# Kernel optimization log

Measured on AMD Instinct MI355X. Metric: run time of the kernel, lower is better.

The kernel has to match this reference:

```python
import jax, jax.numpy as jnp
import numpy as np

N = 50000       # nodes
E = 1600000     # edges (avg degree 32)
F_IN = 128      # input node features
HID = 64        # hidden_dim
H = 2           # heads in conv1
NEG_SLOPE = 0.2 # PyG GATConv default


def gat_conv(x, W, a_src, a_dst, b, src, dst, heads, out_ch):
    """PyG-style GATConv (concat=True). x:[n,f], W:[f,heads*out_ch],
    a_src/a_dst:[heads,out_ch], b:[heads*out_ch], src/dst:[e]."""
    n = x.shape[0]
    xh = (x @ W).reshape(n, heads, out_ch)              # [n,H,C]
    s_src = jnp.sum(xh * a_src[None], axis=-1)          # [n,H]
    s_dst = jnp.sum(xh * a_dst[None], axis=-1)          # [n,H]
    e = jax.nn.leaky_relu(s_src[src] + s_dst[dst], NEG_SLOPE)  # [e,H]
    # segment softmax over incoming edges of each destination node
    emax = jax.ops.segment_max(e, dst, num_segments=n)  # [n,H]
    emax = jnp.where(jnp.isfinite(emax), emax, 0.0)
    p = jnp.exp(e - emax[dst])
    denom = jax.ops.segment_sum(p, dst, num_segments=n)
    alpha = p / (denom[dst] + 1e-16)                    # [e,H]
    out = jax.ops.segment_sum(xh[src] * alpha[..., None], dst, num_segments=n)
    return out.reshape(n, heads * out_ch) + b


def setup_inputs() -> dict:
    key = jax.random.key(0)
    ks = jax.random.split(key, 14)
    g = lambda k, shape, fan: jax.random.normal(k, shape, jnp.float32) / np.sqrt(fan).astype(np.float32)
    return {
        "x": jax.random.normal(ks[0], (N, F_IN), jnp.float32),
        "edge_index": jax.random.randint(ks[1], (2, E), 0, N, jnp.int32),
        "W1": g(ks[2], (F_IN, H * HID), F_IN),
        "a_src1": g(ks[3], (H, HID), HID),
        "a_dst1": g(ks[4], (H, HID), HID),
        "b1": jnp.zeros((H * HID,), jnp.float32),
        "W2": g(ks[5], (H * HID, HID), H * HID),
        "a_src2": g(ks[6], (1, HID), HID),
        "a_dst2": g(ks[7], (1, HID), HID),
        "b2": jnp.zeros((HID,), jnp.float32),
        "Wm": g(ks[8], (HID, 1), HID),
        "bm": jnp.zeros((1,), jnp.float32),
        "Wl": g(ks[9], (HID, 4), HID),
        "bl": jnp.zeros((4,), jnp.float32),
    }


def reference(x, edge_index, W1, a_src1, a_dst1, b1, W2, a_src2, a_dst2, b2, Wm, bm, Wl, bl):
    n = x.shape[0]
    loop = jnp.arange(n, dtype=edge_index.dtype)        # PyG add_self_loops=True
    src = jnp.concatenate([edge_index[0], loop])
    dst = jnp.concatenate([edge_index[1], loop])
    h = jax.nn.relu(gat_conv(x, W1, a_src1, a_dst1, b1, src, dst, H, HID))
    # dropout layers are identity in eval mode
    h = jax.nn.relu(gat_conv(h, W2, a_src2, a_dst2, b2, src, dst, 1, HID))
    mortality = h @ Wm + bm   # [n,1]
    los = h @ Wl + bl         # [n,4]
    return (mortality, los)
```

## Files before the change

kernel.cpp:

```cpp
#include <hip/hip_runtime.h>
#include <hip/hip_bf16.h>

typedef __hip_bfloat16 bf16;
typedef __attribute__((ext_vector_type(8))) short short8;
typedef __attribute__((ext_vector_type(4))) float f32x4;

static __device__ __forceinline__ float lrelu(float x){ return x > 0.f ? x : 0.2f * x; }

static __device__ __forceinline__ float ldf(const void* p, size_t i, int f32){
  return f32 ? ((const float*)p)[i] : __bfloat162float(((const bf16*)p)[i]);
}

static __device__ __forceinline__ float wsum(float v){
#pragma unroll
  for (int o = 32; o; o >>= 1) v += __shfl_xor(v, o, 64);
  return v;
}
static __device__ __forceinline__ float qsum(float v){
  v += __shfl_xor(v, 1); v += __shfl_xor(v, 2);
  v += __shfl_xor(v, 4); v += __shfl_xor(v, 8);
  return v;
}

static __device__ __forceinline__ unsigned short f2bf(float x){
  unsigned u = __float_as_uint(x);
  unsigned r = (u + 0x7fffu + ((u >> 16) & 1u)) >> 16;
  return (unsigned short)r;
}
static __device__ __forceinline__ float bfval(unsigned short h){
  return __uint_as_float(((unsigned)h) << 16);
}
static __device__ __forceinline__ unsigned packbf2(float a, float b){
  return ((unsigned)f2bf(b) << 16) | (unsigned)f2bf(a);
}
static __device__ __forceinline__ float unlo(unsigned v){ return __uint_as_float(v << 16); }
static __device__ __forceinline__ float unhi(unsigned v){ return __uint_as_float(v & 0xffff0000u); }

#define CAP 10240
#define EPB 16
#define CHUNK (256 * EPB)
#define PREPB 96
#define SORTCAP 9216

__global__ __launch_bounds__(256) void k_prep_scatter(
    const unsigned short* __restrict__ xprobe,
    const void* __restrict__ W1, const void* __restrict__ W2,
    int* __restrict__ flag,
    unsigned short* __restrict__ w1hi, unsigned short* __restrict__ w1lo,
    unsigned short* __restrict__ w2hi, unsigned short* __restrict__ w2lo,
    const int* __restrict__ ei, int* __restrict__ bucketCur,
    unsigned* __restrict__ binned, int E, int Etot){
  __shared__ int lcnt[256];
  __shared__ int lcur[256];
  int t = threadIdx.x;
  if (blockIdx.x < PREPB){
    if (t == 0) lcnt[0] = 0;
    __syncthreads();
    int bad = 0;
    for (int i = t; i < 512; i += 256){
      int e = (xprobe[i] >> 7) & 0xFF;
      if (e >= 133) bad++;
    }
    if (bad) atomicAdd(&lcnt[0], bad);
    __syncthreads();
    const int f = lcnt[0] > 8;
    if (blockIdx.x == 0 && t == 0) *flag = f;
    int blk = blockIdx.x;
    const void* W; unsigned short *hi, *lo; int ncol, nct, tg;
    if (blk < 64){ W = W1; hi = w1hi; lo = w1lo; ncol = 128; nct = 8; tg = blk * 256 + t; }
    else         { W = W2; hi = w2hi; lo = w2lo; ncol = 64;  nct = 4; tg = (blk - 64) * 256 + t; }
    int j = tg & 7;
    int lane = (tg >> 3) & 63;
    int ct = (tg >> 9) % nct;
    int kc = tg / (512 * nct);
    int k = kc * 32 + ((lane >> 4) << 3) + j;
    int col = ct * 16 + (lane & 15);
    float w = ldf(W, (size_t)k * ncol + col, f);
    unsigned short h = f2bf(w);
    hi[tg] = h;
    lo[tg] = f2bf(w - bfval(h));
  } else {
    lcnt[t] = 0;
    __syncthreads();
    int base = (blockIdx.x - PREPB) * CHUNK;
    int vsrc[EPB], vdst[EPB];
#pragma unroll
    for (int k = 0; k < EPB; k++){
      int i = base + k * 256 + t;
      vdst[k] = -1;
      if (i < Etot){
        if (i < E){ vsrc[k] = ei[i]; vdst[k] = ei[E + i]; }
        else { vsrc[k] = i - E; vdst[k] = i - E; }
        atomicAdd(&lcnt[vdst[k] >> 8], 1);
      }
    }
    __syncthreads();
    lcur[t] = lcnt[t] ? atomicAdd(&bucketCur[t], lcnt[t]) : 0;
    __syncthreads();
#pragma unroll
    for (int k = 0; k < EPB; k++){
      if (vdst[k] >= 0){
        int b = vdst[k] >> 8;
        int p = atomicAdd(&lcur[b], 1);
        binned[(size_t)b * CAP + p] = (unsigned)vsrc[k] | ((unsigned)(vdst[k] & 255) << 24);
      }
    }
  }
}

__global__ __launch_bounds__(256) void k_sort_gemm1(
    const int* __restrict__ bucketCur, const unsigned* __restrict__ binned,
    int* __restrict__ deg, int* __restrict__ offs, int* __restrict__ csr, int nbuck,
    const void* __restrict__ x,
    const unsigned short* __restrict__ whi, const unsigned short* __restrict__ wlo,
    const void* __restrict__ a_src1, const void* __restrict__ a_dst1,
    const int* __restrict__ flagp,
    unsigned* __restrict__ xh1p, float* __restrict__ ssrc1, float* __restrict__ sdst1, int n){
  __shared__ int smem[768 + SORTCAP];
  int t = threadIdx.x;
  if ((int)blockIdx.x < nbuck){
    int* lcnt = smem;
    int* lsc  = smem + 256;
    int* lcur = smem + 512;
    int* lsrc = smem + 768;
    int b = blockIdx.x;
    int s0 = b * CAP;
    int cnt = bucketCur[b];
    int node0 = b << 8;
    lcnt[t] = 0;
    __syncthreads();
    for (int i = t; i < cnt; i += 256){
      unsigned v = binned[s0 + i];
      atomicAdd(&lcnt[v >> 24], 1);
    }
    __syncthreads();
    lsc[t] = lcnt[t];
    __syncthreads();
#pragma unroll
    for (int o = 1; o < 256; o <<= 1){
      int xv = (t >= o) ? lsc[t - o] : 0;
      __syncthreads();
      lsc[t] += xv;
      __syncthreads();
    }
    int excl = lsc[t] - lcnt[t];
    int node = node0 + t;
    if (node < n){ deg[node] = lcnt[t]; offs[node] = s0 + excl; }
    lcur[t] = excl;
    __syncthreads();
    if (cnt <= SORTCAP){
      for (int i = t; i < cnt; i += 256){
        unsigned v = binned[s0 + i];
        int p = atomicAdd(&lcur[v >> 24], 1);
        lsrc[p] = (int)(v & 0xFFFFFFu);
      }
      __syncthreads();
      for (int i = t; i < cnt; i += 256) csr[s0 + i] = lsrc[i];
    } else {
      for (int i = t; i < cnt; i += 256){
        unsigned v = binned[s0 + i];
        int p = atomicAdd(&lcur[v >> 24], 1);
        csr[s0 + p] = (int)(v & 0xFFFFFFu);
      }
    }
  } else {
    const int f = *flagp;
    int lane = t & 63, w = t >> 6;
    int c16 = lane & 15, quad = lane >> 4;
    int nbw = (blockIdx.x - nbuck) * 64 + w * 16;
    int an = min(nbw + c16, n - 1);
    f32x4 acc[8];
#pragma unroll
    for (int ct = 0; ct < 8; ct++)
#pragma unroll
      for (int r = 0; r < 4; r++) acc[ct][r] = 0.f;

#pragma unroll
    for (int kc = 0; kc < 4; kc++){
      float av[8];
      short8 ahi, alo;
      if (f){
        const float* row = (const float*)x + (size_t)an * 128 + kc * 32 + quad * 8;
        float4 v0 = *(const float4*)row;
        float4 v1 = *(const float4*)(row + 4);
        av[0] = v0.x; av[1] = v0.y; av[2] = v0.z; av[3] = v0.w;
        av[4] = v1.x; av[5] = v1.y; av[6] = v1.z; av[7] = v1.w;
#pragma unroll
        for (int j = 0; j < 8; j++){
          unsigned short h = f2bf(av[j]);
          ahi[j] = (short)h;
          alo[j] = (short)f2bf(av[j] - bfval(h));
        }
      } else {
        const unsigned short* row = (const unsigned short*)x + (size_t)an * 128 + kc * 32 + quad * 8;
        uint4 v = *(const uint4*)row;
        ahi[0] = (short)(v.x & 0xffff); ahi[1] = (short)(v.x >> 16);
        ahi[2] = (short)(v.y & 0xffff); ahi[3] = (short)(v.y >> 16);
        ahi[4] = (short)(v.z & 0xffff); ahi[5] = (short)(v.z >> 16);
        ahi[6] = (short)(v.w & 0xffff); ahi[7] = (short)(v.w >> 16);
#pragma unroll
        for (int j = 0; j < 8; j++) alo[j] = 0;
      }
#pragma unroll
      for (int ct = 0; ct < 8; ct++){
        const short8 bhi = *(const short8*)(whi + (((size_t)(kc * 8 + ct) * 64 + lane) << 3));
        const short8 blo = *(const short8*)(wlo + (((size_t)(kc * 8 + ct) * 64 + lane) << 3));
        acc[ct] = __builtin_amdgcn_mfma_f32_16x16x32_bf16(ahi, blo, acc[ct], 0, 0, 0);
        acc[ct] = __builtin_amdgcn_mfma_f32_16x16x32_bf16(alo, bhi, acc[ct], 0, 0, 0);
        acc[ct] = __builtin_amdgcn_mfma_f32_16x16x32_bf16(ahi, bhi, acc[ct], 0, 0, 0);
      }
    }

    float as[8], ad[8];
#pragma unroll
    for (int ct = 0; ct < 8; ct++){
      as[ct] = ldf(a_src1, ct * 16 + c16, f);
      ad[ct] = ldf(a_dst1, ct * 16 + c16, f);
    }
    float vs0[4], vs1[4], vd0[4], vd1[4];
#pragma unroll
    for (int r = 0; r < 4; r++){
      float s0 = 0.f, s1 = 0.f, d0 = 0.f, d1 = 0.f;
#pragma unroll
      for (int ct = 0; ct < 4; ct++){
        s0 += acc[ct][r] * as[ct];         d0 += acc[ct][r] * ad[ct];
        s1 += acc[ct + 4][r] * as[ct + 4]; d1 += acc[ct + 4][r] * ad[ct + 4];
      }
      vs0[r] = qsum(s0); vs1[r] = qsum(s1);
      vd0[r] = qsum(d0); vd1[r] = qsum(d1);
    }
#pragma unroll
    for (int r = 0; r < 4; r++){
      int node = nbw + quad * 4 + r;
      if (node < n){
#pragma unroll
        for (int ct = 0; ct < 4; ct++)
          xh1p[(size_t)node * 64 + ct * 16 + c16] = packbf2(acc[ct][r], acc[ct + 4][r]);
      }
    }
    if (c16 == 0){
#pragma unroll
      for (int r = 0; r < 4; r++){
        int node = nbw + quad * 4 + r;
        if (node < n){
          ssrc1[node * 2]     = vs0[r];
          ssrc1[node * 2 + 1] = vs1[r];
          sdst1[node * 2]     = vd0[r];
          sdst1[node * 2 + 1] = vd1[r];
        }
      }
    }
  }
}

__global__ __launch_bounds__(256) void k_gemm2m(
    const unsigned* __restrict__ h1p,
    const unsigned short* __restrict__ whi, const unsigned short* __restrict__ wlo,
    const void* __restrict__ a_src2, const void* __restrict__ a_dst2,
    const int* __restrict__ flagp,
    unsigned short* __restrict__ xh2b, float* __restrict__ ssrc2, float* __restrict__ sdst2, int n){
  const int f = *flagp;
  int t = threadIdx.x;
  int lane = t & 63, w = t >> 6;
  int c16 = lane & 15, quad = lane >> 4;
  int nbw = blockIdx.x * 64 + w * 16;
  int an = min(nbw + c16, n - 1);
  f32x4 acc[4];
#pragma unroll
  for (int ct = 0; ct < 4; ct++)
#pragma unroll
    for (int r = 0; r < 4; r++) acc[ct][r] = 0.f;

#pragma unroll
  for (int kc = 0; kc < 4; kc++){
    const uint4* hp = (const uint4*)h1p;
    uint4 v = hp[(size_t)an * 16 + kc * 4 + quad];
    short8 ahi;
    ahi[0] = (short)(v.x & 0xffff); ahi[1] = (short)(v.x >> 16);
    ahi[2] = (short)(v.y & 0xffff); ahi[3] = (short)(v.y >> 16);
    ahi[4] = (short)(v.z & 0xffff); ahi[5] = (short)(v.z >> 16);
    ahi[6] = (short)(v.w & 0xffff); ahi[7] = (short)(v.w >> 16);
#pragma unroll
    for (int ct = 0; ct < 4; ct++){
      const short8 bhi = *(const short8*)(whi + (((size_t)(kc * 4 + ct) * 64 + lane) << 3));
      const short8 blo = *(const short8*)(wlo + (((size_t)(kc * 4 + ct) * 64 + lane) << 3));
      acc[ct] = __builtin_amdgcn_mfma_f32_16x16x32_bf16(ahi, blo, acc[ct], 0, 0, 0);
      acc[ct] = __builtin_amdgcn_mfma_f32_16x16x32_bf16(ahi, bhi, acc[ct], 0, 0, 0);
    }
  }

  float as[4], ad[4];
#pragma unroll
  for (int ct = 0; ct < 4; ct++){
    as[ct] = ldf(a_src2, ct * 16 + c16, f);
    ad[ct] = ldf(a_dst2, ct * 16 + c16, f);
  }
  float vs[4], vd[4];
#pragma unroll
  for (int r = 0; r < 4; r++){
    float s = 0.f, d = 0.f;
#pragma unroll
    for (int ct = 0; ct < 4; ct++){
      s += acc[ct][r] * as[ct];
      d += acc[ct][r] * ad[ct];
    }
    vs[r] = qsum(s); vd[r] = qsum(d);
  }
#pragma unroll
  for (int r = 0; r < 4; r++){
    int node = nbw + quad * 4 + r;
    if (node < n){
#pragma unroll
      for (int ct = 0; ct < 4; ct++)
        xh2b[(size_t)node * 64 + ct * 16 + c16] = f2bf(acc[ct][r]);
    }
  }
  if (c16 == 0){
#pragma unroll
    for (int r = 0; r < 4; r++){
      int node = nbw + quad * 4 + r;
      if (node < n){ ssrc2[node] = vs[r]; sdst2[node] = vd[r]; }
    }
  }
}

__global__ __launch_bounds__(256) void k_agg1(
    const int* __restrict__ offs, const int* __restrict__ deg, const int* __restrict__ csr,
    const float2* __restrict__ ssrc, const float2* __restrict__ sdst,
    const unsigned* __restrict__ xh1p, const void* __restrict__ b1,
    const int* __restrict__ flagp, unsigned* __restrict__ h1p, int n){
  __shared__ float4 stg[4][64];
  int wv = threadIdx.x >> 6;
  int wid = (int)(((size_t)blockIdx.x * blockDim.x + threadIdx.x) >> 6);
  int lane = threadIdx.x & 63;
  if (wid >= n) return;
  int st = offs[wid], d = deg[wid];
  int half = lane >> 5, u = lane & 31;
  float2 sd = sdst[wid];
  const char* __restrict__ xb = (const char*)xh1p;
  const unsigned uoff = (unsigned)u * 8u;
  float Z0l = 0.f, Z1l = 0.f;
  float a0x = 0.f, a0y = 0.f, a1x = 0.f, a1y = 0.f;
  for (int base = 0; base < d; base += 64){
    int idx = base + lane;
    bool val = idx < d;
    int s = csr[st + (val ? idx : 0)];
    float2 sv = ssrc[s];
    float e0 = fminf(lrelu(sv.x + sd.x), 80.f);
    float e1 = fminf(lrelu(sv.y + sd.y), 80.f);
    float p0 = val ? __expf(e0) : 0.f;
    float p1 = val ? __expf(e1) : 0.f;
    Z0l += p0; Z1l += p1;
    float4 tv; tv.x = __uint_as_float((unsigned)s); tv.y = p0; tv.z = p1; tv.w = 0.f;
    stg[wv][lane] = tv;
    int cnt = min(64, d - base);
    int pairs = (cnt + 1) >> 1;
    for (int pj = 0; pj < pairs; pj += 8){
      unsigned offv[8]; float q0v[8], q1v[8]; uint2 vv[8];
#pragma unroll
      for (int k = 0; k < 8; k++){
        int jj = ((pj + k) << 1) + half;
        float4 v = stg[wv][jj];
        offv[k] = (__float_as_uint(v.x) << 8) + uoff;
        q0v[k] = v.y;
        q1v[k] = v.z;
      }
#pragma unroll
      for (int k = 0; k < 8; k++)
        vv[k] = *(const uint2*)(xb + offv[k]);
#pragma unroll
      for (int k = 0; k < 8; k++){
        a0x = fmaf(q0v[k], unlo(vv[k].x), a0x); a0y = fmaf(q0v[k], unlo(vv[k].y), a0y);
        a1x = fmaf(q1v[k], unhi(vv[k].x), a1x); a1y = fmaf(q1v[k], unhi(vv[k].y), a1y);
      }
    }
  }
  a0x += __shfl_xor(a0x, 32); a0y += __shfl_xor(a0y, 32);
  a1x += __shfl_xor(a1x, 32); a1y += __shfl_xor(a1y, 32);
  float Z0 = wsum(Z0l), Z1 = wsum(Z1l);
  const int f = *flagp;
  float Zh = half ? Z1 : Z0;
  float ax = half ? a1x : a0x;
  float ay = half ? a1y : a0y;
  float inv = 1.f / (Zh + 1e-16f);
  float bx = ldf(b1, half * 64 + 2 * u, f);
  float by = ldf(b1, half * 64 + 2 * u + 1, f);
  float ox = fmaxf(ax * inv + bx, 0.f);
  float oy = fmaxf(ay * inv + by, 0.f);
  h1p[(size_t)wid * 64 + half * 32 + u] = packbf2(ox, oy);
}

__global__ __launch_bounds__(256) void k_agg2(
    const int* __restrict__ offs, const int* __restrict__ deg, const int* __restrict__ csr,
    const float* __restrict__ ssrc, const float* __restrict__ sdstA,
    const unsigned short* __restrict__ xh2b, const void* __restrict__ bias2,
    const void* __restrict__ Wm, const void* __restrict__ bm,
    const void* __restrict__ Wlos, const void* __restrict__ bl,
    const int* __restrict__ flagp, void* __restrict__ out, int n){
  __shared__ float2 stg[4][96];
  int wv = threadIdx.x >> 6;
  int wid = (int)(((size_t)blockIdx.x * blockDim.x + threadIdx.x) >> 6);
  int lane = threadIdx.x & 63;
  if (wid >= n) return;
  int st = offs[wid], d = deg[wid];
  int half = lane >> 5, u = lane & 31;
  if (lane < 32){ float2 z; z.x = __uint_as_float(0u); z.y = 0.f; stg[wv][64 + lane] = z; }
  float sd = sdstA[wid];
  const char* __restrict__ xb = (const char*)xh2b;
  const unsigned uoff = (unsigned)u * 4u;
  float Zl = 0.f, ax = 0.f, ay = 0.f;
  for (int base = 0; base < d; base += 64){
    int idx = base + lane;
    bool val = idx < d;
    int s = csr[st + (val ? idx : 0)];
    float e = fminf(lrelu(ssrc[s] + sd), 80.f);
    float p = val ? __expf(e) : 0.f;
    Zl += p;
    float2 tv; tv.x = __uint_as_float((unsigned)s); tv.y = p;
    stg[wv][lane] = tv;
    int cnt = min(64, d - base);
    int pairs = (cnt + 1) >> 1;
    for (int pj = 0; pj < pairs; pj += 12){
      unsigned offv[12]; float qv[12]; unsigned vv[12];
#pragma unroll
      for (int k = 0; k < 12; k++){
        int jj = ((pj + k) << 1) + half;
        float2 v = stg[wv][jj];
        offv[k] = (__float_as_uint(v.x) << 7) + uoff;
        qv[k] = v.y;
      }
#pragma unroll
      for (int k = 0; k < 12; k++)
        vv[k] = *(const unsigned*)(xb + offv[k]);
#pragma unroll
      for (int k = 0; k < 12; k++){
        ax = fmaf(qv[k], unlo(vv[k]), ax);
        ay = fmaf(qv[k], unhi(vv[k]), ay);
      }
    }
  }
  ax += __shfl_xor(ax, 32);
  ay += __shfl_xor(ay, 32);
  float Z = wsum(Zl);
  const int f = *flagp;
  float inv = 1.f / (Z + 1e-16f);
  float hx = fmaxf(ax * inv + ldf(bias2, 2 * u, f), 0.f);
  float hy = fmaxf(ay * inv + ldf(bias2, 2 * u + 1, f), 0.f);
  bool lo32 = (half == 0);
  float mo = wsum(lo32 ? hx * ldf(Wm, 2 * u, f) + hy * ldf(Wm, 2 * u + 1, f) : 0.f);
  float l0 = wsum(lo32 ? hx * ldf(Wlos, (2 * u) * 4 + 0, f) + hy * ldf(Wlos, (2 * u + 1) * 4 + 0, f) : 0.f);
  float l1 = wsum(lo32 ? hx * ldf(Wlos, (2 * u) * 4 + 1, f) + hy * ldf(Wlos, (2 * u + 1) * 4 + 1, f) : 0.f);
  float l2 = wsum(lo32 ? hx * ldf(Wlos, (2 * u) * 4 + 2, f) + hy * ldf(Wlos, (2 * u + 1) * 4 + 2, f) : 0.f);
  float l3 = wsum(lo32 ? hx * ldf(Wlos, (2 * u) * 4 + 3, f) + hy * ldf(Wlos, (2 * u + 1) * 4 + 3, f) : 0.f);
  if (lane == 0){
    float vm = mo + ldf(bm, 0, f);
    float v0 = l0 + ldf(bl, 0, f);
    float v1 = l1 + ldf(bl, 1, f);
    float v2 = l2 + ldf(bl, 2, f);
    float v3 = l3 + ldf(bl, 3, f);
    if (f){
      float* o = (float*)out;
      o[wid] = vm;
      float4 lv = make_float4(v0, v1, v2, v3);
      *(float4*)&o[n + wid * 4] = lv;
    } else {
      bf16* o = (bf16*)out;
      o[wid] = __float2bfloat16(vm);
      o[n + wid * 4 + 0] = __float2bfloat16(v0); o[n + wid * 4 + 1] = __float2bfloat16(v1);
      o[n + wid * 4 + 2] = __float2bfloat16(v2); o[n + wid * 4 + 3] = __float2bfloat16(v3);
    }
  }
}

extern "C" void kernel_launch(void* const* d_in, const int* in_sizes, int n_in,
                              void* d_out, int out_size, void* d_ws, size_t ws_size,
                              hipStream_t stream){
  const void* x      = d_in[0];
  const int*  ei     = (const int*)d_in[1];
  const void* W1     = d_in[2];
  const void* a_src1 = d_in[3];
  const void* a_dst1 = d_in[4];
  const void* b1     = d_in[5];
  const void* W2     = d_in[6];
  const void* a_src2 = d_in[7];
  const void* a_dst2 = d_in[8];
  const void* bias2  = d_in[9];
  const void* Wm     = d_in[10];
  const void* bm     = d_in[11];
  const void* Wlos   = d_in[12];
  const void* bl     = d_in[13];

  const int N = in_sizes[0] / 128;
  const int E = in_sizes[1] / 2;
  const int Etot = E + N;
  const int NBUCK = (N + 255) >> 8;

  char* base = (char*)d_ws;
  size_t off = 0;
  auto alloc = [&](size_t bytes) -> void* {
    void* r = base + off;
    off += (bytes + 255) & ~(size_t)255;
    return r;
  };
  int*      flag  = (int*)alloc(256);
  unsigned* xh1p  = (unsigned*)alloc((size_t)N * 64 * 4);
  unsigned* h1p   = (unsigned*)alloc((size_t)N * 64 * 4);
  float*    ssrc1 = (float*)alloc((size_t)N * 2 * 4);
  float*    sdst1 = (float*)alloc((size_t)N * 2 * 4);
  float*    ssrc2 = (float*)alloc((size_t)N * 4);
  float*    sdst2 = (float*)alloc((size_t)N * 4);
  int*      deg    = (int*)alloc((size_t)N * 4);
  int*      offsb  = (int*)alloc((size_t)N * 4);
  unsigned* binned = (unsigned*)alloc((size_t)NBUCK * CAP * 4);
  int*      csr    = (int*)alloc((size_t)NBUCK * CAP * 4);
  int*      bucketCur = (int*)alloc(1024);
  unsigned short* w1hi = (unsigned short*)alloc(16384 * 2);
  unsigned short* w1lo = (unsigned short*)alloc(16384 * 2);
  unsigned short* w2hi = (unsigned short*)alloc(8192 * 2);
  unsigned short* w2lo = (unsigned short*)alloc(8192 * 2);
  unsigned short* xh2b = (unsigned short*)xh1p;

  const int nchunk = (Etot + CHUNK - 1) / CHUNK;
  const int ngemm1 = (N + 63) / 64;

  hipMemsetAsync(bucketCur, 0, (size_t)NBUCK * 4, stream);

  k_prep_scatter<<<PREPB + nchunk, 256, 0, stream>>>(
      (const unsigned short*)x, W1, W2, flag, w1hi, w1lo, w2hi, w2lo,
      ei, bucketCur, binned, E, Etot);

  k_sort_gemm1<<<NBUCK + ngemm1, 256, 0, stream>>>(
      bucketCur, binned, deg, offsb, csr, NBUCK,
      x, w1hi, w1lo, a_src1, a_dst1, flag, xh1p, ssrc1, sdst1, N);

  k_agg1<<<(N + 3) / 4, 256, 0, stream>>>(offsb, deg, csr, (const float2*)ssrc1, (const float2*)sdst1,
                                          xh1p, b1, flag, h1p, N);

  k_gemm2m<<<(N + 63) / 64, 256, 0, stream>>>(h1p, w2hi, w2lo, a_src2, a_dst2, flag, xh2b, ssrc2, sdst2, N);
  k_agg2<<<(N + 3) / 4, 256, 0, stream>>>(offsb, deg, csr, ssrc2, sdst2, xh2b, bias2,
                                          Wm, bm, Wlos, bl, flag, d_out, N);
}
```

Measured before the change: 258.1 us.

## Split aggregation waves into quarter-waves with wide gathers and double-buffered loads

Both edge-aggregation kernels now give each quarter-wave its own edge, so every lane gathers 16 bytes (layer 1) or 8 bytes (layer 2) of the source row instead of 8 or 4. Loads for the next group of 16 edges are issued before the current group's FMAs run, a manual double-buffering meant to hide gather latency. Partial sums are reduced across quarters at the end, and launch bounds now request 8 blocks per CU. This targets latency and instruction overhead in the memory-bound gathers, at the cost of more registers per lane and an extra shuffle reduction.

```diff
diff --git a/kernel.cpp b/kernel.cpp
--- a/kernel.cpp
+++ b/kernel.cpp
@@ -324,7 +324,23 @@
   }
 }
 
-__global__ __launch_bounds__(256) void k_agg1(
+#define AG1_ISSUE(V0,V1,V2,V3,P) { \
+  int b0_ = ((P) << 4) + qd; \
+  V0 = *(const uint4*)(xb + ((__float_as_uint(stg[wv][b0_ +  0].x) << 8) + uoff)); \
+  V1 = *(const uint4*)(xb + ((__float_as_uint(stg[wv][b0_ +  4].x) << 8) + uoff)); \
+  V2 = *(const uint4*)(xb + ((__float_as_uint(stg[wv][b0_ +  8].x) << 8) + uoff)); \
+  V3 = *(const uint4*)(xb + ((__float_as_uint(stg[wv][b0_ + 12].x) << 8) + uoff)); }
+#define AG1_FMA1(V,SL) { \
+  float4 w_ = stg[wv][SL]; float q0_ = w_.y, q1_ = w_.z; \
+  a00 = fmaf(q0_, unlo(V.x), a00); a10 = fmaf(q1_, unhi(V.x), a10); \
+  a01 = fmaf(q0_, unlo(V.y), a01); a11 = fmaf(q1_, unhi(V.y), a11); \
+  a02 = fmaf(q0_, unlo(V.z), a02); a12 = fmaf(q1_, unhi(V.z), a12); \
+  a03 = fmaf(q0_, unlo(V.w), a03); a13 = fmaf(q1_, unhi(V.w), a13); }
+#define AG1_CONSUME(V0,V1,V2,V3,P) { \
+  int c0_ = ((P) << 4) + qd; \
+  AG1_FMA1(V0, c0_ + 0) AG1_FMA1(V1, c0_ + 4) AG1_FMA1(V2, c0_ + 8) AG1_FMA1(V3, c0_ + 12) }
+
+__global__ __launch_bounds__(256, 8) void k_agg1(
     const int* __restrict__ offs, const int* __restrict__ deg, const int* __restrict__ csr,
     const float2* __restrict__ ssrc, const float2* __restrict__ sdst,
     const unsigned* __restrict__ xh1p, const void* __restrict__ b1,
@@ -335,12 +351,13 @@
   int lane = threadIdx.x & 63;
   if (wid >= n) return;
   int st = offs[wid], d = deg[wid];
-  int half = lane >> 5, u = lane & 31;
+  int u16 = lane & 15, qd = lane >> 4;
   float2 sd = sdst[wid];
   const char* __restrict__ xb = (const char*)xh1p;
-  const unsigned uoff = (unsigned)u * 8u;
+  const unsigned uoff = (unsigned)u16 * 16u;
   float Z0l = 0.f, Z1l = 0.f;
-  float a0x = 0.f, a0y = 0.f, a1x = 0.f, a1y = 0.f;
+  float a00 = 0.f, a01 = 0.f, a02 = 0.f, a03 = 0.f;
+  float a10 = 0.f, a11 = 0.f, a12 = 0.f, a13 = 0.f;
   for (int base = 0; base < d; base += 64){
     int idx = base + lane;
     bool val = idx < d;
@@ -354,104 +371,121 @@
     float4 tv; tv.x = __uint_as_float((unsigned)s); tv.y = p0; tv.z = p1; tv.w = 0.f;
     stg[wv][lane] = tv;
     int cnt = min(64, d - base);
-    int pairs = (cnt + 1) >> 1;
-    for (int pj = 0; pj < pairs; pj += 8){
-      unsigned offv[8]; float q0v[8], q1v[8]; uint2 vv[8];
-#pragma unroll
-      for (int k = 0; k < 8; k++){
-        int jj = ((pj + k) << 1) + half;
-        float4 v = stg[wv][jj];
-        offv[k] = (__float_as_uint(v.x) << 8) + uoff;
-        q0v[k] = v.y;
-        q1v[k] = v.z;
-      }
-#pragma unroll
-      for (int k = 0; k < 8; k++)
-        vv[k] = *(const uint2*)(xb + offv[k]);
-#pragma unroll
-      for (int k = 0; k < 8; k++){
-        a0x = fmaf(q0v[k], unlo(vv[k].x), a0x); a0y = fmaf(q0v[k], unlo(vv[k].y), a0y);
-        a1x = fmaf(q1v[k], unhi(vv[k].x), a1x); a1y = fmaf(q1v[k], unhi(vv[k].y), a1y);
-      }
-    }
-  }
-  a0x += __shfl_xor(a0x, 32); a0y += __shfl_xor(a0y, 32);
-  a1x += __shfl_xor(a1x, 32); a1y += __shfl_xor(a1y, 32);
+    int nph = (cnt + 15) >> 4;
+    uint4 vA0, vA1, vA2, vA3, vB0, vB1, vB2, vB3;
+    AG1_ISSUE(vA0, vA1, vA2, vA3, 0)
+    int ph = 0;
+    for (; ph + 1 < nph; ph++){
+      if (ph & 1){ AG1_ISSUE(vA0, vA1, vA2, vA3, ph + 1) AG1_CONSUME(vB0, vB1, vB2, vB3, ph) }
+      else       { AG1_ISSUE(vB0, vB1, vB2, vB3, ph + 1) AG1_CONSUME(vA0, vA1, vA2, vA3, ph) }
+    }
+    if (ph & 1){ AG1_CONSUME(vB0, vB1, vB2, vB3, ph) }
+    else       { AG1_CONSUME(vA0, vA1, vA2, vA3, ph) }
+  }
+  a00 += __shfl_xor(a00, 16); a00 += __shfl_xor(a00, 32);
+  a01 += __shfl_xor(a01, 16); a01 += __shfl_xor(a01, 32);
+  a02 += __shfl_xor(a02, 16); a02 += __shfl_xor(a02, 32);
+  a03 += __shfl_xor(a03, 16); a03 += __shfl_xor(a03, 32);
+  a10 += __shfl_xor(a10, 16); a10 += __shfl_xor(a10, 32);
+  a11 += __shfl_xor(a11, 16); a11 += __shfl_xor(a11, 32);
+  a12 += __shfl_xor(a12, 16); a12 += __shfl_xor(a12, 32);
+  a13 += __shfl_xor(a13, 16); a13 += __shfl_xor(a13, 32);
   float Z0 = wsum(Z0l), Z1 = wsum(Z1l);
   const int f = *flagp;
-  float Zh = half ? Z1 : Z0;
-  float ax = half ? a1x : a0x;
-  float ay = half ? a1y : a0y;
-  float inv = 1.f / (Zh + 1e-16f);
-  float bx = ldf(b1, half * 64 + 2 * u, f);
-  float by = ldf(b1, half * 64 + 2 * u + 1, f);
-  float ox = fmaxf(ax * inv + bx, 0.f);
-  float oy = fmaxf(ay * inv + by, 0.f);
-  h1p[(size_t)wid * 64 + half * 32 + u] = packbf2(ox, oy);
-}
-
-__global__ __launch_bounds__(256) void k_agg2(
+  if (qd < 2){
+    float Zh = qd ? Z1 : Z0;
+    float inv = 1.f / (Zh + 1e-16f);
+    float v0 = qd ? a10 : a00;
+    float v1 = qd ? a11 : a01;
+    float v2 = qd ? a12 : a02;
+    float v3 = qd ? a13 : a03;
+    int c0 = qd * 64 + 4 * u16;
+    float h0 = fmaxf(v0 * inv + ldf(b1, c0 + 0, f), 0.f);
+    float h1 = fmaxf(v1 * inv + ldf(b1, c0 + 1, f), 0.f);
+    float h2 = fmaxf(v2 * inv + ldf(b1, c0 + 2, f), 0.f);
+    float h3 = fmaxf(v3 * inv + ldf(b1, c0 + 3, f), 0.f);
+    uint2 w; w.x = packbf2(h0, h1); w.y = packbf2(h2, h3);
+    *(uint2*)((char*)h1p + (size_t)wid * 256 + (unsigned)(qd * 128 + u16 * 8)) = w;
+  }
+}
+
+#define AG2_ISSUE(V0,V1,V2,V3,P) { \
+  int b0_ = ((P) << 4) + qd; \
+  V0 = *(const uint2*)(xb + ((__float_as_uint(stg[wv][b0_ +  0].x) << 7) + uoff)); \
+  V1 = *(const uint2*)(xb + ((__float_as_uint(stg[wv][b0_ +  4].x) << 7) + uoff)); \
+  V2 = *(const uint2*)(xb + ((__float_as_uint(stg[wv][b0_ +  8].x) << 7) + uoff)); \
+  V3 = *(const uint2*)(xb + ((__float_as_uint(stg[wv][b0_ + 12].x) << 7) + uoff)); }
+#define AG2_FMA1(V,SL) { \
+  float2 w_ = stg[wv][SL]; float q_ = w_.y; \
+  c0a = fmaf(q_, unlo(V.x), c0a); c1a = fmaf(q_, unhi(V.x), c1a); \
+  c2a = fmaf(q_, unlo(V.y), c2a); c3a = fmaf(q_, unhi(V.y), c3a); }
+#define AG2_CONSUME(V0,V1,V2,V3,P) { \
+  int c0_ = ((P) << 4) + qd; \
+  AG2_FMA1(V0, c0_ + 0) AG2_FMA1(V1, c0_ + 4) AG2_FMA1(V2, c0_ + 8) AG2_FMA1(V3, c0_ + 12) }
+
+__global__ __launch_bounds__(256, 8) void k_agg2(
     const int* __restrict__ offs, const int* __restrict__ deg, const int* __restrict__ csr,
     const float* __restrict__ ssrc, const float* __restrict__ sdstA,
     const unsigned short* __restrict__ xh2b, const void* __restrict__ bias2,
     const void* __restrict__ Wm, const void* __restrict__ bm,
     const void* __restrict__ Wlos, const void* __restrict__ bl,
     const int* __restrict__ flagp, void* __restrict__ out, int n){
-  __shared__ float2 stg[4][96];
+  __shared__ float2 stg[4][64];
   int wv = threadIdx.x >> 6;
   int wid = (int)(((size_t)blockIdx.x * blockDim.x + threadIdx.x) >> 6);
   int lane = threadIdx.x & 63;
   if (wid >= n) return;
   int st = offs[wid], d = deg[wid];
-  int half = lane >> 5, u = lane & 31;
-  if (lane < 32){ float2 z; z.x = __uint_as_float(0u); z.y = 0.f; stg[wv][64 + lane] = z; }
+  int u16 = lane & 15, qd = lane >> 4;
   float sd = sdstA[wid];
   const char* __restrict__ xb = (const char*)xh2b;
-  const unsigned uoff = (unsigned)u * 4u;
-  float Zl = 0.f, ax = 0.f, ay = 0.f;
+  const unsigned uoff = (unsigned)u16 * 8u;
+  float Zl = 0.f;
+  float c0a = 0.f, c1a = 0.f, c2a = 0.f, c3a = 0.f;
   for (int base = 0; base < d; base += 64){
     int idx = base + lane;
     bool val = idx < d;
     int s = csr[st + (val ? idx : 0)];
     float e = fminf(lrelu(ssrc[s] + sd), 80.f);
-    float p = val ? __expf(e) : 0.f;
-    Zl += p;
-    float2 tv; tv.x = __uint_as_float((unsigned)s); tv.y = p;
+    float pw = val ? __expf(e) : 0.f;
+    Zl += pw;
+    float2 tv; tv.x = __uint_as_float((unsigned)s); tv.y = pw;
     stg[wv][lane] = tv;
     int cnt = min(64, d - base);
-    int pairs = (cnt + 1) >> 1;
-    for (int pj = 0; pj < pairs; pj += 12){
-      unsigned offv[12]; float qv[12]; unsigned vv[12];
-#pragma unroll
-      for (int k = 0; k < 12; k++){
-        int jj = ((pj + k) << 1) + half;
-        float2 v = stg[wv][jj];
-        offv[k] = (__float_as_uint(v.x) << 7) + uoff;
-        qv[k] = v.y;
-      }
-#pragma unroll
-      for (int k = 0; k < 12; k++)
-        vv[k] = *(const unsigned*)(xb + offv[k]);
-#pragma unroll
-      for (int k = 0; k < 12; k++){
-        ax = fmaf(qv[k], unlo(vv[k]), ax);
-        ay = fmaf(qv[k], unhi(vv[k]), ay);
-      }
-    }
-  }
-  ax += __shfl_xor(ax, 32);
-  ay += __shfl_xor(ay, 32);
+    int nph = (cnt + 15) >> 4;
+    uint2 vA0, vA1, vA2, vA3, vB0, vB1, vB2, vB3;
+    AG2_ISSUE(vA0, vA1, vA2, vA3, 0)
+    int ph = 0;
+    for (; ph + 1 < nph; ph++){
+      if (ph & 1){ AG2_ISSUE(vA0, vA1, vA2, vA3, ph + 1) AG2_CONSUME(vB0, vB1, vB2, vB3, ph) }
+      else       { AG2_ISSUE(vB0, vB1, vB2, vB3, ph + 1) AG2_CONSUME(vA0, vA1, vA2, vA3, ph) }
+    }
+    if (ph & 1){ AG2_CONSUME(vB0, vB1, vB2, vB3, ph) }
+    else       { AG2_CONSUME(vA0, vA1, vA2, vA3, ph) }
+  }
+  c0a += __shfl_xor(c0a, 16); c0a += __shfl_xor(c0a, 32);
+  c1a += __shfl_xor(c1a, 16); c1a += __shfl_xor(c1a, 32);
+  c2a += __shfl_xor(c2a, 16); c2a += __shfl_xor(c2a, 32);
+  c3a += __shfl_xor(c3a, 16); c3a += __shfl_xor(c3a, 32);
   float Z = wsum(Zl);
   const int f = *flagp;
   float inv = 1.f / (Z + 1e-16f);
-  float hx = fmaxf(ax * inv + ldf(bias2, 2 * u, f), 0.f);
-  float hy = fmaxf(ay * inv + ldf(bias2, 2 * u + 1, f), 0.f);
-  bool lo32 = (half == 0);
-  float mo = wsum(lo32 ? hx * ldf(Wm, 2 * u, f) + hy * ldf(Wm, 2 * u + 1, f) : 0.f);
-  float l0 = wsum(lo32 ? hx * ldf(Wlos, (2 * u) * 4 + 0, f) + hy * ldf(Wlos, (2 * u + 1) * 4 + 0, f) : 0.f);
-  float l1 = wsum(lo32 ? hx * ldf(Wlos, (2 * u) * 4 + 1, f) + hy * ldf(Wlos, (2 * u + 1) * 4 + 1, f) : 0.f);
-  float l2 = wsum(lo32 ? hx * ldf(Wlos, (2 * u) * 4 + 2, f) + hy * ldf(Wlos, (2 * u + 1) * 4 + 2, f) : 0.f);
-  float l3 = wsum(lo32 ? hx * ldf(Wlos, (2 * u) * 4 + 3, f) + hy * ldf(Wlos, (2 * u + 1) * 4 + 3, f) : 0.f);
+  int cch = 4 * u16;
+  float h0 = fmaxf(c0a * inv + ldf(bias2, cch + 0, f), 0.f);
+  float h1 = fmaxf(c1a * inv + ldf(bias2, cch + 1, f), 0.f);
+  float h2 = fmaxf(c2a * inv + ldf(bias2, cch + 2, f), 0.f);
+  float h3 = fmaxf(c3a * inv + ldf(bias2, cch + 3, f), 0.f);
+  bool qz = (qd == 0);
+  float mo = wsum(qz ? h0 * ldf(Wm, cch, f) + h1 * ldf(Wm, cch + 1, f)
+                     + h2 * ldf(Wm, cch + 2, f) + h3 * ldf(Wm, cch + 3, f) : 0.f);
+  float l0 = wsum(qz ? h0 * ldf(Wlos, cch * 4 + 0, f) + h1 * ldf(Wlos, (cch + 1) * 4 + 0, f)
+                     + h2 * ldf(Wlos, (cch + 2) * 4 + 0, f) + h3 * ldf(Wlos, (cch + 3) * 4 + 0, f) : 0.f);
+  float l1 = wsum(qz ? h0 * ldf(Wlos, cch * 4 + 1, f) + h1 * ldf(Wlos, (cch + 1) * 4 + 1, f)
+                     + h2 * ldf(Wlos, (cch + 2) * 4 + 1, f) + h3 * ldf(Wlos, (cch + 3) * 4 + 1, f) : 0.f);
+  float l2 = wsum(qz ? h0 * ldf(Wlos, cch * 4 + 2, f) + h1 * ldf(Wlos, (cch + 1) * 4 + 2, f)
+                     + h2 * ldf(Wlos, (cch + 2) * 4 + 2, f) + h3 * ldf(Wlos, (cch + 3) * 4 + 2, f) : 0.f);
+  float l3 = wsum(qz ? h0 * ldf(Wlos, cch * 4 + 3, f) + h1 * ldf(Wlos, (cch + 1) * 4 + 3, f)
+                     + h2 * ldf(Wlos, (cch + 2) * 4 + 3, f) + h3 * ldf(Wlos, (cch + 3) * 4 + 3, f) : 0.f);
   if (lane == 0){
     float vm = mo + ldf(bm, 0, f);
     float v0 = l0 + ldf(bl, 0, f);
```

After: 302.7 us. 1.17x slower.
